# Performance work log

Measured on AMD Instinct MI355X. Metric: run time of the kernel, lower is better.

The kernel has to match this reference:

```python
import jax, jax.numpy as jnp
import numpy as np

N, T, DS, DD = 20000, 8, 16, 8   # nodes, seq_len, static dim, dynamic dim
E = 320000                        # edges (before self loops)
HL = 128                          # LSTM hidden
GH, GC = 4, 128                   # GAT heads, channels per head
HC = GH * GC                      # 512 concat output
EMB = 64
IN1 = DS + HL                     # layer-1 GNN input dim (static + lstm)


def setup_inputs() -> dict:
    ks = jax.random.split(jax.random.key(0), 20)
    p = lambda k, s: jax.random.normal(k, s, jnp.float32) * 0.05
    return {
        "x_static": jax.random.normal(ks[0], (N, DS), jnp.float32),
        "dynamic_seq": jax.random.normal(ks[1], (N, T, DD), jnp.float32),
        "edge_index": jax.random.randint(ks[2], (2, E), 0, N),
        # LSTM params (PyTorch gate order i,f,g,o)
        "W_ih": p(ks[3], (4 * HL, DD)), "W_hh": p(ks[4], (4 * HL, HL)),
        "b_ih": p(ks[5], (4 * HL,)), "b_hh": p(ks[6], (4 * HL,)),
        # GATv2 layer 1
        "Wl1": p(ks[7], (HC, IN1)), "Wr1": p(ks[8], (HC, IN1)),
        "att1": p(ks[9], (GH, GC)), "bg1": p(ks[10], (HC,)),
        # GATv2 layer 2
        "Wl2": p(ks[11], (HC, HC)), "Wr2": p(ks[12], (HC, HC)),
        "att2": p(ks[13], (GH, GC)), "bg2": p(ks[14], (HC,)),
        # BatchNorm affine params
        "gamma1": jnp.ones((HC,), jnp.float32), "beta1": jnp.zeros((HC,), jnp.float32),
        "gamma2": jnp.ones((HC,), jnp.float32), "beta2": jnp.zeros((HC,), jnp.float32),
        # output projection
        "Wp": p(ks[15], (EMB, HC)), "bp": p(ks[16], (EMB,)),
    }


def _lstm(seq, W_ih, W_hh, b_ih, b_hh):
    """Single-layer LSTM over [N, T, DD] -> [T, N, HL]."""
    n = seq.shape[0]
    b = b_ih + b_hh

    def step(carry, x_t):
        h, c = carry
        g = x_t @ W_ih.T + h @ W_hh.T + b            # [N, 4*HL]
        i, f, gg, o = jnp.split(g, 4, axis=-1)
        c = jax.nn.sigmoid(f) * c + jax.nn.sigmoid(i) * jnp.tanh(gg)
        h = jax.nn.sigmoid(o) * jnp.tanh(c)
        return (h, c), h

    h0 = jnp.zeros((n, HL), seq.dtype)
    _, hs = jax.lax.scan(step, (h0, h0), jnp.swapaxes(seq, 0, 1))
    return hs


def _gatv2(x, src, dst, Wl, Wr, att, bias):
    """GATv2Conv (concat heads, self-loops already in src/dst, eval dropout)."""
    xl = (x @ Wl.T).reshape(N, GH, GC)   # source transform
    xr = (x @ Wr.T).reshape(N, GH, GC)   # target transform
    e = jax.nn.leaky_relu(xl[src] + xr[dst], 0.2)       # [E', GH, GC]
    s = jnp.einsum('ehc,hc->eh', e, att)                # [E', GH]
    smax = jax.ops.segment_max(s, dst, num_segments=N)  # scatter-softmax (stable)
    ex = jnp.exp(s - smax[dst])
    den = jax.ops.segment_sum(ex, dst, num_segments=N)
    alpha = ex / den[dst]
    out = jax.ops.segment_sum(alpha[:, :, None] * xl[src], dst, num_segments=N)
    return out.reshape(N, HC) + bias


def _bn(x, g, b):
    m = x.mean(0)
    v = x.var(0)
    return (x - m) * jax.lax.rsqrt(v + 1e-5) * g + b


def reference(x_static, dynamic_seq, edge_index, W_ih, W_hh, b_ih, b_hh,
              Wl1, Wr1, att1, bg1, Wl2, Wr2, att2, bg2,
              gamma1, beta1, gamma2, beta2, Wp, bp):
    loops = jnp.arange(N)
    src = jnp.concatenate([edge_index[0], loops])  # add self loops (PyG default)
    dst = jnp.concatenate([edge_index[1], loops])
    hs = _lstm(dynamic_seq, W_ih, W_hh, b_ih, b_hh)  # [T, N, HL]

    def step(_, h_t):
        g = jnp.concatenate([x_static, h_t], axis=1)                 # [N, IN1]
        g = jax.nn.relu(_bn(_gatv2(g, src, dst, Wl1, Wr1, att1, bg1), gamma1, beta1))
        g = jax.nn.relu(_bn(_gatv2(g, src, dst, Wl2, Wr2, att2, bg2), gamma2, beta2))
        return None, g @ Wp.T + bp                                   # [N, EMB]

    _, emb = jax.lax.scan(step, None, hs)  # [T, N, EMB]
    return jnp.swapaxes(emb, 0, 1)         # [N, T, EMB]
```

## Files before the change

kernel.cpp:

```cpp
#include <hip/hip_runtime.h>
#include <math.h>

typedef unsigned short u16;
typedef unsigned int u32;

#define N_NODES 20000
#define MP      20480
#define T_SEQ   8
#define DS      16
#define DD      8
#define E_EDGES 320000
#define HL      128
#define GH      4
#define GC      128
#define HC      512
#define EMB     64
#define KP1     160
#define EP      (E_EDGES + N_NODES)

typedef __attribute__((ext_vector_type(8))) short bf16x8;
typedef __attribute__((ext_vector_type(4))) float f32x4;

__device__ __forceinline__ u16 f2bf(float f) {
  u32 u = __float_as_uint(f);
  u += 0x7fff + ((u >> 16) & 1);
  return (u16)(u >> 16);
}
__device__ __forceinline__ float bflo(u32 v) { return __uint_as_float(v << 16); }
__device__ __forceinline__ float bfhi(u32 v) { return __uint_as_float(v & 0xffff0000u); }

__device__ __forceinline__ void gld16(const void* g, void* l) {
  __builtin_amdgcn_global_load_lds(
      (const __attribute__((address_space(1))) void*)g,
      (__attribute__((address_space(3))) void*)l, 16, 0, 0);
}

__device__ __forceinline__ float rowsum16(float p) {
  p += __int_as_float(__builtin_amdgcn_update_dpp(0, __float_as_int(p), 0x121, 0xf, 0xf, false));
  p += __int_as_float(__builtin_amdgcn_update_dpp(0, __float_as_int(p), 0x122, 0xf, 0xf, false));
  p += __int_as_float(__builtin_amdgcn_update_dpp(0, __float_as_int(p), 0x124, 0xf, 0xf, false));
  p += __int_as_float(__builtin_amdgcn_update_dpp(0, __float_as_int(p), 0x128, 0xf, 0xf, false));
  return p;
}

__global__ __launch_bounds__(256) void gemm_mfma(
    const u16* __restrict__ A, int lda,
    const u16* __restrict__ W, int ldw,
    const float* __restrict__ bias,
    void* __restrict__ Cout, int ldc,
    int M, int Nc, int K, int c_bf16, int gxs)
{
  __shared__ u16 smem[16384];
  u16* Asm = smem;
  u16* Bsm = smem + 8192;

  const int tid = threadIdx.x;
  const int wave = tid >> 6, lane = tid & 63;
  const int wm = (wave >> 1) << 6, wn = (wave & 1) << 6;

  const u32 id = blockIdx.x;
  const int xcd = id & 7;
  const u32 sl = id >> 3;
  const int GXm = (1 << gxs) - 1;
  const int bn = (int)(sl & GXm) << 7;
  const int bm = (xcd + (int)((sl >> gxs) << 3)) << 7;

  f32x4 acc[4][4];
#pragma unroll
  for (int i = 0; i < 4; ++i)
#pragma unroll
    for (int j = 0; j < 4; ++j) acc[i][j] = (f32x4){0.f, 0.f, 0.f, 0.f};

  const int qr = lane >> 2;
  const int qc = (lane & 3) << 3;
  const int q0 = wave * 2, q1 = wave * 2 + 1;
  const int ra0 = bm + q0 * 16 + qr;
  const int ra1 = bm + q1 * 16 + qr;
  int rb0 = bn + q0 * 16 + qr; if (rb0 >= Nc) rb0 = Nc - 1;
  int rb1 = bn + q1 * 16 + qr; if (rb1 >= Nc) rb1 = Nc - 1;

  const u16* pa0 = A + (size_t)ra0 * lda + qc;
  const u16* pa1 = A + (size_t)ra1 * lda + qc;
  const u16* pb0 = W + (size_t)rb0 * ldw + qc;
  const u16* pb1 = W + (size_t)rb1 * ldw + qc;

  const int fm = lane & 15;
  const int fk = (lane >> 4) << 3;

  gld16(pa0, &Asm[q0 * 512]);
  gld16(pa1, &Asm[q1 * 512]);
  gld16(pb0, &Bsm[q0 * 512]);
  gld16(pb1, &Bsm[q1 * 512]);
  pa0 += 32; pa1 += 32; pb0 += 32; pb1 += 32;

  const int iters = K >> 5;
#pragma unroll 2
  for (int it = 0; it < iters; ++it) {
    const int cur = (it & 1) * 4096;
    __syncthreads();
    if (it + 1 < iters) {
      const int nxt = cur ^ 4096;
      gld16(pa0, &Asm[nxt + q0 * 512]);
      gld16(pa1, &Asm[nxt + q1 * 512]);
      gld16(pb0, &Bsm[nxt + q0 * 512]);
      gld16(pb1, &Bsm[nxt + q1 * 512]);
      pa0 += 32; pa1 += 32; pb0 += 32; pb1 += 32;
    }
    bf16x8 af[4], bfr[4];
#pragma unroll
    for (int i = 0; i < 4; ++i)
      af[i] = *(const bf16x8*)&Asm[cur + (wm + i * 16 + fm) * 32 + fk];
#pragma unroll
    for (int j = 0; j < 4; ++j)
      bfr[j] = *(const bf16x8*)&Bsm[cur + (wn + j * 16 + fm) * 32 + fk];
#pragma unroll
    for (int i = 0; i < 4; ++i)
#pragma unroll
      for (int j = 0; j < 4; ++j)
        acc[i][j] = __builtin_amdgcn_mfma_f32_16x16x32_bf16(af[i], bfr[j], acc[i][j], 0, 0, 0);
  }

  const int cn = lane & 15, cm = (lane >> 4) << 2;
  if (c_bf16) {
    __syncthreads();
#pragma unroll
    for (int j = 0; j < 4; ++j) {
      const int c = wn + j * 16 + cn;
      const float bb = bias ? bias[bn + c] : 0.f;
#pragma unroll
      for (int i = 0; i < 4; ++i) {
#pragma unroll
        for (int r = 0; r < 4; ++r)
          smem[(wm + i * 16 + cm + r) * 128 + c] = f2bf(acc[i][j][r] + bb);
      }
    }
    __syncthreads();
    u16* outc = (u16*)Cout;
#pragma unroll
    for (int k = 0; k < 8; ++k) {
      const int idx = tid + k * 256;
      const int r = idx >> 4, cc = (idx & 15) << 3;
      *(uint4*)(outc + (size_t)(bm + r) * ldc + bn + cc) = *(const uint4*)&smem[r * 128 + cc];
    }
  } else {
#pragma unroll
    for (int j = 0; j < 4; ++j) {
      const int c = bn + wn + j * 16 + cn;
      if (c >= Nc) continue;
      const float bb = bias ? bias[c] : 0.f;
#pragma unroll
      for (int i = 0; i < 4; ++i) {
#pragma unroll
        for (int r = 0; r < 4; ++r) {
          const int m = bm + wm + i * 16 + cm + r;
          if (m >= M) continue;
          ((float*)Cout)[(size_t)m * ldc + c] = acc[i][j][r] + bb;
        }
      }
    }
  }
}

__global__ void k_bias_sum(const float* __restrict__ b_ih,
                           const float* __restrict__ b_hh,
                           float* __restrict__ bsum) {
  int i = blockIdx.x * blockDim.x + threadIdx.x;
  if (i < 4 * HL) bsum[i] = b_ih[i] + b_hh[i];
}

__global__ void k_wcat_bf(const float* __restrict__ W_ih,
                          const float* __restrict__ W_hh,
                          u16* __restrict__ w) {
  int idx = blockIdx.x * blockDim.x + threadIdx.x;
  if (idx >= HC * KP1) return;
  int j = idx / KP1, k = idx - j * KP1;
  float v = 0.f;
  if (k < DD) v = W_ih[j * DD + k];
  else if (k < DD + HL) v = W_hh[j * HL + (k - DD)];
  w[idx] = f2bf(v);
}

__global__ void k_wlr1_bf(const float* __restrict__ Wl,
                          const float* __restrict__ Wr,
                          u16* __restrict__ w) {
  int idx = blockIdx.x * blockDim.x + threadIdx.x;
  if (idx >= 2 * HC * KP1) return;
  int j = idx / KP1, k = idx - j * KP1;
  const float* src = (j < HC) ? Wl : Wr;
  int jj = j & (HC - 1);
  float v = (k < DS + HL) ? src[jj * (DS + HL) + k] : 0.f;
  w[idx] = f2bf(v);
}

__global__ void k_wlr2_bf(const float* __restrict__ Wl,
                          const float* __restrict__ Wr,
                          u16* __restrict__ w) {
  int idx = blockIdx.x * blockDim.x + threadIdx.x;
  if (idx >= 2 * HC * HC) return;
  int j = idx >> 9, k = idx & (HC - 1);
  const float* src = (j < HC) ? Wl : Wr;
  int jj = j & (HC - 1);
  w[idx] = f2bf(src[jj * HC + k]);
}

__global__ void k_wp_bf(const float* __restrict__ Wp, u16* __restrict__ w) {
  int idx = blockIdx.x * blockDim.x + threadIdx.x;
  if (idx < EMB * HC) w[idx] = f2bf(Wp[idx]);
}

__global__ void k_pack_static(const float* __restrict__ xs, u16* __restrict__ packG1) {
  int idx = blockIdx.x * blockDim.x + threadIdx.x;
  if (idx >= N_NODES * DS) return;
  int n = idx >> 4, k = idx & 15;
  packG1[(size_t)n * KP1 + k] = f2bf(xs[idx]);
}

__global__ void k_pack_dyn(const float* __restrict__ dyn, u16* __restrict__ packXH) {
  int idx = blockIdx.x * blockDim.x + threadIdx.x;
  if (idx >= N_NODES * DD) return;
  int n = idx >> 3, k = idx & 7;
  packXH[(size_t)n * KP1 + k] = f2bf(dyn[(size_t)n * (T_SEQ * DD) + k]);
}

__global__ void lstm_update(const float* __restrict__ gates,
                            float* __restrict__ c,
                            u16* __restrict__ packXH, u16* __restrict__ packG1,
                            const float* __restrict__ dyn, int t_next) {
  int idx = blockIdx.x * blockDim.x + threadIdx.x;
  if (idx >= N_NODES * HL) return;
  int n = idx >> 7, j = idx & 127;
  const float* g = gates + (size_t)n * HC;
  float gi = g[j], gf = g[j + 128], gg = g[j + 256], go = g[j + 384];
  float si = 1.f / (1.f + __expf(-gi));
  float sf = 1.f / (1.f + __expf(-gf));
  float so = 1.f / (1.f + __expf(-go));
  float cn = sf * c[idx] + si * tanhf(gg);
  c[idx] = cn;
  u16 hb = f2bf(so * tanhf(cn));
  packXH[(size_t)n * KP1 + DD + j] = hb;
  packG1[(size_t)n * KP1 + DS + j] = hb;
  if (j < DD && t_next < T_SEQ)
    packXH[(size_t)n * KP1 + j] =
        f2bf(dyn[(size_t)n * (T_SEQ * DD) + t_next * DD + j]);
}

__global__ void k_deg(const int* __restrict__ ei, int* __restrict__ deg) {
  int e = blockIdx.x * blockDim.x + threadIdx.x;
  if (e >= EP) return;
  int d = (e < E_EDGES) ? ei[E_EDGES + e] : (e - E_EDGES);
  atomicAdd(&deg[d], 1);
}

__global__ __launch_bounds__(1024) void k_scan(const int* __restrict__ deg,
                                               int* __restrict__ rowstart) {
  __shared__ int buf[1024];
  __shared__ int carry_s;
  const int tid = threadIdx.x;
  if (tid == 0) carry_s = 0;
  __syncthreads();
  for (int base = 0; base < N_NODES; base += 1024) {
    int v = (base + tid < N_NODES) ? deg[base + tid] : 0;
    buf[tid] = v;
    __syncthreads();
    for (int off = 1; off < 1024; off <<= 1) {
      int add = (tid >= off) ? buf[tid - off] : 0;
      __syncthreads();
      buf[tid] += add;
      __syncthreads();
    }
    int incl = buf[tid];
    int carry = carry_s;
    if (base + tid < N_NODES) rowstart[base + tid] = carry + incl - v;
    __syncthreads();
    if (tid == 1023) carry_s = carry + incl;
    __syncthreads();
  }
  if (tid == 0) rowstart[N_NODES] = carry_s;
}

__global__ void k_fill(const int* __restrict__ ei,
                       const int* __restrict__ rowstart,
                       int* __restrict__ cursor, int* __restrict__ csr) {
  int e = blockIdx.x * blockDim.x + threadIdx.x;
  if (e >= EP) return;
  int s, d;
  if (e < E_EDGES) { s = ei[e]; d = ei[E_EDGES + e]; }
  else             { s = d = e - E_EDGES; }
  int pos = atomicAdd(&cursor[d], 1);
  csr[rowstart[d] + pos] = s;
}

__global__ __launch_bounds__(256) void gat_edge(
    const u16* __restrict__ xlr,
    const float* __restrict__ att, const float* __restrict__ bias,
    const int* __restrict__ rowstart, const int* __restrict__ csr,
    u16* __restrict__ outb)
{
  const int wave = threadIdx.x >> 6, lane = threadIdx.x & 63;
  const int d = blockIdx.x * 4 + wave;
  const int ch = lane * 8;
  const uint4 vr = *(const uint4*)(xlr + (size_t)d * 1024 + 512 + ch);
  const float rxa0 = bflo(vr.x), rxa1 = bfhi(vr.x), rxa2 = bflo(vr.y), rxa3 = bfhi(vr.y);
  const float rxb0 = bflo(vr.z), rxb1 = bfhi(vr.z), rxb2 = bflo(vr.w), rxb3 = bfhi(vr.w);
  const float4 ava = *(const float4*)(att + ch);
  const float4 avb = *(const float4*)(att + ch + 4);
  const int row = rowstart[d], end = rowstart[d + 1];
  const char* __restrict__ xbase = (const char*)(xlr + ch);

  float l = 0.f;
  float a0 = 0.f, a1 = 0.f, a2 = 0.f, a3 = 0.f;
  float b0 = 0.f, b1 = 0.f, b2 = 0.f, b3 = 0.f;

#define GAT_STEP(v)                                                          \
  {                                                                          \
    const float xa0 = bflo((v).x), xa1 = bfhi((v).x);                        \
    const float xa2 = bflo((v).y), xa3 = bfhi((v).y);                        \
    const float xb0 = bflo((v).z), xb1 = bfhi((v).z);                        \
    const float xb2 = bflo((v).w), xb3 = bfhi((v).w);                        \
    const float e0 = xa0 + rxa0, e1 = xa1 + rxa1;                            \
    const float e2 = xa2 + rxa2, e3 = xa3 + rxa3;                            \
    const float f0 = xb0 + rxb0, f1 = xb1 + rxb1;                            \
    const float f2 = xb2 + rxb2, f3 = xb3 + rxb3;                            \
    float ps = e0 * ava.x;                                                   \
    ps = fmaf(e1, ava.y, ps); ps = fmaf(e2, ava.z, ps);                      \
    ps = fmaf(e3, ava.w, ps); ps = fmaf(f0, avb.x, ps);                      \
    ps = fmaf(f1, avb.y, ps); ps = fmaf(f2, avb.z, ps);                      \
    ps = fmaf(f3, avb.w, ps);                                                \
    float pa = fabsf(e0) * ava.x;                                            \
    pa = fmaf(fabsf(e1), ava.y, pa); pa = fmaf(fabsf(e2), ava.z, pa);        \
    pa = fmaf(fabsf(e3), ava.w, pa); pa = fmaf(fabsf(f0), avb.x, pa);        \
    pa = fmaf(fabsf(f1), avb.y, pa); pa = fmaf(fabsf(f2), avb.z, pa);        \
    pa = fmaf(fabsf(f3), avb.w, pa);                                         \
    float p = rowsum16(fmaf(0.6f, ps, 0.4f * pa));                           \
    const float w = __expf(p);                                               \
    l += w;                                                                  \
    a0 = fmaf(w, xa0, a0); a1 = fmaf(w, xa1, a1);                            \
    a2 = fmaf(w, xa2, a2); a3 = fmaf(w, xa3, a3);                            \
    b0 = fmaf(w, xb0, b0); b1 = fmaf(w, xb1, b1);                            \
    b2 = fmaf(w, xb2, b2); b3 = fmaf(w, xb3, b3);                            \
  }

  int i = row;
  for (; i + 3 < end; i += 4) {
    const u32 s0 = (u32)csr[i],     s1 = (u32)csr[i + 1];
    const u32 s2 = (u32)csr[i + 2], s3 = (u32)csr[i + 3];
    const uint4 v0 = *(const uint4*)(xbase + (s0 << 11));
    const uint4 v1 = *(const uint4*)(xbase + (s1 << 11));
    const uint4 v2 = *(const uint4*)(xbase + (s2 << 11));
    const uint4 v3 = *(const uint4*)(xbase + (s3 << 11));
    GAT_STEP(v0);
    GAT_STEP(v1);
    GAT_STEP(v2);
    GAT_STEP(v3);
  }
  for (; i < end; ++i) {
    const u32 s0 = (u32)csr[i];
    const uint4 v0 = *(const uint4*)(xbase + (s0 << 11));
    GAT_STEP(v0);
  }
#undef GAT_STEP

  const float inv = 1.f / l;
  const float4 ba = *(const float4*)(bias + ch);
  const float4 bb = *(const float4*)(bias + ch + 4);
  uint4 ov;
  ov.x = (u32)f2bf(fmaf(a0, inv, ba.x)) | ((u32)f2bf(fmaf(a1, inv, ba.y)) << 16);
  ov.y = (u32)f2bf(fmaf(a2, inv, ba.z)) | ((u32)f2bf(fmaf(a3, inv, ba.w)) << 16);
  ov.z = (u32)f2bf(fmaf(b0, inv, bb.x)) | ((u32)f2bf(fmaf(b1, inv, bb.y)) << 16);
  ov.w = (u32)f2bf(fmaf(b2, inv, bb.z)) | ((u32)f2bf(fmaf(b3, inv, bb.w)) << 16);
  *(uint4*)(outb + (size_t)d * HC + ch) = ov;
}

__global__ __launch_bounds__(256) void bn_stats(const u16* __restrict__ x,
                                                float* __restrict__ stats) {
  const int tid = threadIdx.x;
  const int rows_per = (N_NODES + gridDim.x - 1) / gridDim.x;
  const int r0 = blockIdx.x * rows_per;
  const int r1 = min(r0 + rows_per, N_NODES);
  const u32* xp = (const u32*)x;
  float s0 = 0.f, s1 = 0.f, q0 = 0.f, q1 = 0.f;
  for (int r = r0; r < r1; ++r) {
    const u32 v = xp[(size_t)r * 256 + tid];
    const float v0 = bflo(v), v1 = bfhi(v);
    s0 += v0; q0 += v0 * v0;
    s1 += v1; q1 += v1 * v1;
  }
  atomicAdd(&stats[2 * tid],          s0);
  atomicAdd(&stats[2 * tid + 1],      s1);
  atomicAdd(&stats[HC + 2 * tid],     q0);
  atomicAdd(&stats[HC + 2 * tid + 1], q1);
}

__global__ void bn_apply(const u16* __restrict__ x, const float* __restrict__ stats,
                         const float* __restrict__ gamma, const float* __restrict__ beta,
                         u16* __restrict__ outb) {
  int idx = blockIdx.x * blockDim.x + threadIdx.x;
  if (idx >= N_NODES * (HC / 2)) return;
  const int cc = idx & (HC / 2 - 1);
  const int c0 = cc * 2, c1 = c0 + 1;
  const u32 v = ((const u32*)x)[idx];
  const float mean0 = stats[c0] * (1.f / N_NODES);
  const float mean1 = stats[c1] * (1.f / N_NODES);
  const float inv0 = rsqrtf(stats[HC + c0] * (1.f / N_NODES) - mean0 * mean0 + 1e-5f);
  const float inv1 = rsqrtf(stats[HC + c1] * (1.f / N_NODES) - mean1 * mean1 + 1e-5f);
  float z0 = (bflo(v) - mean0) * inv0 * gamma[c0] + beta[c0];
  float z1 = (bfhi(v) - mean1) * inv1 * gamma[c1] + beta[c1];
  z0 = z0 > 0.f ? z0 : 0.f;
  z1 = z1 > 0.f ? z1 : 0.f;
  ((u32*)outb)[idx] = (u32)f2bf(z0) | ((u32)f2bf(z1) << 16);
}

extern "C" void kernel_launch(void* const* d_in, const int* in_sizes, int n_in,
                              void* d_out, int out_size, void* d_ws, size_t ws_size,
                              hipStream_t stream) {
  const float* x_static = (const float*)d_in[0];
  const float* dyn      = (const float*)d_in[1];
  const int*   ei       = (const int*)d_in[2];
  const float* W_ih     = (const float*)d_in[3];
  const float* W_hh     = (const float*)d_in[4];
  const float* b_ih     = (const float*)d_in[5];
  const float* b_hh     = (const float*)d_in[6];
  const float* Wl1      = (const float*)d_in[7];
  const float* Wr1      = (const float*)d_in[8];
  const float* att1     = (const float*)d_in[9];
  const float* bg1      = (const float*)d_in[10];
  const float* Wl2      = (const float*)d_in[11];
  const float* Wr2      = (const float*)d_in[12];
  const float* att2     = (const float*)d_in[13];
  const float* bg2      = (const float*)d_in[14];
  const float* gamma1   = (const float*)d_in[15];
  const float* beta1    = (const float*)d_in[16];
  const float* gamma2   = (const float*)d_in[17];
  const float* beta2    = (const float*)d_in[18];
  const float* Wp       = (const float*)d_in[19];
  const float* bp       = (const float*)d_in[20];
  float* out = (float*)d_out;

  float* ws = (float*)d_ws;
  size_t o = 0;
  float* c     = ws + o; o += (size_t)MP * HL;
  float* gates = ws + o; o += (size_t)MP * HC;
  float* stats = ws + o; o += 4 * HC;
  float* bsum  = ws + o; o += 4 * HL;
  u16* packXH  = (u16*)(ws + o); o += (size_t)MP * KP1 / 2;
  u16* packG1  = (u16*)(ws + o); o += (size_t)MP * KP1 / 2;
  u16* xlr     = (u16*)(ws + o); o += (size_t)MP * 1024 / 2;
  u16* gout    = (u16*)(ws + o); o += (size_t)MP * HC / 2;
  u16* aggb    = (u16*)(ws + o); o += (size_t)MP * HC / 2;
  u16* wcat_bf = (u16*)(ws + o); o += (size_t)HC * KP1 / 2;
  u16* wlr1_bf = (u16*)(ws + o); o += (size_t)2 * HC * KP1 / 2;
  u16* wlr2_bf = (u16*)(ws + o); o += (size_t)2 * HC * HC / 2;
  u16* wp_bf   = (u16*)(ws + o); o += (size_t)EMB * HC / 2;
  int* deg      = (int*)(ws + o); o += N_NODES;
  int* cursor   = (int*)(ws + o); o += N_NODES;
  int* rowstart = (int*)(ws + o); o += N_NODES + 64;
  int* csr      = (int*)(ws + o); o += EP;

  hipMemsetAsync(deg,    0, N_NODES * sizeof(int), stream);
  hipMemsetAsync(cursor, 0, N_NODES * sizeof(int), stream);
  hipMemsetAsync(c,      0, (size_t)MP * HL * sizeof(float), stream);
  hipMemsetAsync(packXH, 0, (size_t)MP * KP1 * sizeof(u16), stream);
  hipMemsetAsync(packG1, 0, (size_t)MP * KP1 * sizeof(u16), stream);
  hipMemsetAsync(aggb,   0, (size_t)MP * HC * sizeof(u16), stream);

  k_bias_sum<<<2, 256, 0, stream>>>(b_ih, b_hh, bsum);
  k_wcat_bf<<<(HC * KP1 + 255) / 256, 256, 0, stream>>>(W_ih, W_hh, wcat_bf);
  k_wlr1_bf<<<(2 * HC * KP1 + 255) / 256, 256, 0, stream>>>(Wl1, Wr1, wlr1_bf);
  k_wlr2_bf<<<(2 * HC * HC + 255) / 256, 256, 0, stream>>>(Wl2, Wr2, wlr2_bf);
  k_wp_bf<<<(EMB * HC + 255) / 256, 256, 0, stream>>>(Wp, wp_bf);
  k_pack_static<<<(N_NODES * DS + 255) / 256, 256, 0, stream>>>(x_static, packG1);
  k_pack_dyn<<<(N_NODES * DD + 255) / 256, 256, 0, stream>>>(dyn, packXH);
  k_deg<<<(EP + 255) / 256, 256, 0, stream>>>(ei, deg);
  k_scan<<<1, 1024, 0, stream>>>(deg, rowstart);
  k_fill<<<(EP + 255) / 256, 256, 0, stream>>>(ei, rowstart, cursor, csr);

  const int GY = MP / 128;

  for (int t = 0; t < T_SEQ; ++t) {
    gemm_mfma<<<4 * GY, 256, 0, stream>>>(packXH, KP1, wcat_bf, KP1, bsum,
                                          gates, HC, MP, HC, KP1, 0, 2);
    lstm_update<<<(N_NODES * HL + 255) / 256, 256, 0, stream>>>(
        gates, c, packXH, packG1, dyn, t + 1);

    hipMemsetAsync(stats, 0, 4 * HC * sizeof(float), stream);

    gemm_mfma<<<8 * GY, 256, 0, stream>>>(packG1, KP1, wlr1_bf, KP1, nullptr,
                                          xlr, 1024, MP, 2 * HC, KP1, 1, 3);
    gat_edge<<<N_NODES / 4, 256, 0, stream>>>(xlr, att1, bg1, rowstart, csr, gout);
    bn_stats<<<500, 256, 0, stream>>>(gout, stats);
    bn_apply<<<(N_NODES * HC / 2 + 255) / 256, 256, 0, stream>>>(gout, stats,
                                                                 gamma1, beta1, aggb);

    gemm_mfma<<<8 * GY, 256, 0, stream>>>(aggb, HC, wlr2_bf, HC, nullptr,
                                          xlr, 1024, MP, 2 * HC, HC, 1, 3);
    gat_edge<<<N_NODES / 4, 256, 0, stream>>>(xlr, att2, bg2, rowstart, csr, gout);
    bn_stats<<<500, 256, 0, stream>>>(gout, stats + 2 * HC);
    bn_apply<<<(N_NODES * HC / 2 + 255) / 256, 256, 0, stream>>>(gout, stats + 2 * HC,
                                                                 gamma2, beta2, aggb);

    gemm_mfma<<<1 * GY, 256, 0, stream>>>(aggb, HC, wp_bf, HC, bp,
                                          out + t * EMB, T_SEQ * EMB,
                                          N_NODES, EMB, HC, 0, 0);
  }
}
```

Before: 2.501 ms.

## Pad CSR rows to multiples of four and software-pipeline GAT edge gathers

Each CSR row is padded to a multiple of four entries with masked dummy edges, and source indices are stored pre-shifted. This lets the GAT edge loop drop its remainder loop and prefetch the next group of four neighbour rows while computing the current one. Separately, LSTM gate pre-activations are now written in bf16 rather than fp32 to cut memory traffic. Per-step BN stats memsets are hoisted into one upfront memset. Padding adds wasted gather work, and bf16 gates reduce precision in the LSTM recurrence.

```diff
diff --git a/kernel.cpp b/kernel.cpp
--- a/kernel.cpp
+++ b/kernel.cpp
@@ -17,6 +17,7 @@
 #define EMB     64
 #define KP1     160
 #define EP      (E_EDGES + N_NODES)
+#define EPP     (EP + 3 * N_NODES)
 
 typedef __attribute__((ext_vector_type(8))) short bf16x8;
 typedef __attribute__((ext_vector_type(4))) float f32x4;
@@ -28,6 +29,7 @@
 }
 __device__ __forceinline__ float bflo(u32 v) { return __uint_as_float(v << 16); }
 __device__ __forceinline__ float bfhi(u32 v) { return __uint_as_float(v & 0xffff0000u); }
+__device__ __forceinline__ float bf16f(u16 v) { return __uint_as_float((u32)v << 16); }
 
 __device__ __forceinline__ void gld16(const void* g, void* l) {
   __builtin_amdgcn_global_load_lds(
@@ -222,15 +224,16 @@
   packXH[(size_t)n * KP1 + k] = f2bf(dyn[(size_t)n * (T_SEQ * DD) + k]);
 }
 
-__global__ void lstm_update(const float* __restrict__ gates,
+__global__ void lstm_update(const u16* __restrict__ gatesb,
                             float* __restrict__ c,
                             u16* __restrict__ packXH, u16* __restrict__ packG1,
                             const float* __restrict__ dyn, int t_next) {
   int idx = blockIdx.x * blockDim.x + threadIdx.x;
   if (idx >= N_NODES * HL) return;
   int n = idx >> 7, j = idx & 127;
-  const float* g = gates + (size_t)n * HC;
-  float gi = g[j], gf = g[j + 128], gg = g[j + 256], go = g[j + 384];
+  const u16* g = gatesb + (size_t)n * HC;
+  float gi = bf16f(g[j]), gf = bf16f(g[j + 128]);
+  float gg = bf16f(g[j + 256]), go = bf16f(g[j + 384]);
   float si = 1.f / (1.f + __expf(-gi));
   float sf = 1.f / (1.f + __expf(-gf));
   float so = 1.f / (1.f + __expf(-go));
@@ -259,7 +262,7 @@
   if (tid == 0) carry_s = 0;
   __syncthreads();
   for (int base = 0; base < N_NODES; base += 1024) {
-    int v = (base + tid < N_NODES) ? deg[base + tid] : 0;
+    int v = (base + tid < N_NODES) ? ((deg[base + tid] + 3) & ~3) : 0;
     buf[tid] = v;
     __syncthreads();
     for (int off = 1; off < 1024; off <<= 1) {
@@ -280,20 +283,29 @@
 
 __global__ void k_fill(const int* __restrict__ ei,
                        const int* __restrict__ rowstart,
-                       int* __restrict__ cursor, int* __restrict__ csr) {
+                       int* __restrict__ cursor, u32* __restrict__ csr) {
   int e = blockIdx.x * blockDim.x + threadIdx.x;
   if (e >= EP) return;
   int s, d;
   if (e < E_EDGES) { s = ei[e]; d = ei[E_EDGES + e]; }
   else             { s = d = e - E_EDGES; }
   int pos = atomicAdd(&cursor[d], 1);
-  csr[rowstart[d] + pos] = s;
+  csr[rowstart[d] + pos] = (u32)s << 11;
+}
+
+__global__ void k_pad(const int* __restrict__ deg,
+                      const int* __restrict__ rowstart, u32* __restrict__ csr) {
+  int d = blockIdx.x * blockDim.x + threadIdx.x;
+  if (d >= N_NODES) return;
+  int s = rowstart[d] + deg[d], e = rowstart[d + 1];
+  const u32 pv = ((u32)d << 11) | 1;
+  for (int i = s; i < e; ++i) csr[i] = pv;
 }
 
 __global__ __launch_bounds__(256) void gat_edge(
     const u16* __restrict__ xlr,
     const float* __restrict__ att, const float* __restrict__ bias,
-    const int* __restrict__ rowstart, const int* __restrict__ csr,
+    const int* __restrict__ rowstart, const u32* __restrict__ csr,
     u16* __restrict__ outb)
 {
   const int wave = threadIdx.x >> 6, lane = threadIdx.x & 63;
@@ -311,7 +323,9 @@
   float a0 = 0.f, a1 = 0.f, a2 = 0.f, a3 = 0.f;
   float b0 = 0.f, b1 = 0.f, b2 = 0.f, b3 = 0.f;
 
-#define GAT_STEP(v)                                                          \
+#define GLD(o) (*(const uint4*)(xbase + (size_t)((o) & ~1u)))
+
+#define GAT_STEP(v, o)                                                       \
   {                                                                          \
     const float xa0 = bflo((v).x), xa1 = bfhi((v).x);                        \
     const float xa2 = bflo((v).y), xa3 = bfhi((v).y);                        \
@@ -332,7 +346,8 @@
     pa = fmaf(fabsf(f1), avb.y, pa); pa = fmaf(fabsf(f2), avb.z, pa);        \
     pa = fmaf(fabsf(f3), avb.w, pa);                                         \
     float p = rowsum16(fmaf(0.6f, ps, 0.4f * pa));                           \
-    const float w = __expf(p);                                               \
+    float w = __expf(p);                                                     \
+    w = ((o) & 1) ? 0.f : w;                                                 \
     l += w;                                                                  \
     a0 = fmaf(w, xa0, a0); a1 = fmaf(w, xa1, a1);                            \
     a2 = fmaf(w, xa2, a2); a3 = fmaf(w, xa3, a3);                            \
@@ -340,25 +355,29 @@
     b2 = fmaf(w, xb2, b2); b3 = fmaf(w, xb3, b3);                            \
   }
 
-  int i = row;
-  for (; i + 3 < end; i += 4) {
-    const u32 s0 = (u32)csr[i],     s1 = (u32)csr[i + 1];
-    const u32 s2 = (u32)csr[i + 2], s3 = (u32)csr[i + 3];
-    const uint4 v0 = *(const uint4*)(xbase + (s0 << 11));
-    const uint4 v1 = *(const uint4*)(xbase + (s1 << 11));
-    const uint4 v2 = *(const uint4*)(xbase + (s2 << 11));
-    const uint4 v3 = *(const uint4*)(xbase + (s3 << 11));
-    GAT_STEP(v0);
-    GAT_STEP(v1);
-    GAT_STEP(v2);
-    GAT_STEP(v3);
-  }
-  for (; i < end; ++i) {
-    const u32 s0 = (u32)csr[i];
-    const uint4 v0 = *(const uint4*)(xbase + (s0 << 11));
-    GAT_STEP(v0);
-  }
+  const u32* cp = csr + row;
+  const int nq = (end - row) >> 2;
+
+  u32 o0 = cp[0], o1 = cp[1], o2 = cp[2], o3 = cp[3];
+  uint4 v0 = GLD(o0), v1 = GLD(o1), v2 = GLD(o2), v3 = GLD(o3);
+
+  for (int q = 1; q < nq; ++q) {
+    cp += 4;
+    const u32 n0 = cp[0], n1 = cp[1], n2 = cp[2], n3 = cp[3];
+    const uint4 w0 = GLD(n0), w1 = GLD(n1), w2 = GLD(n2), w3 = GLD(n3);
+    GAT_STEP(v0, o0);
+    GAT_STEP(v1, o1);
+    GAT_STEP(v2, o2);
+    GAT_STEP(v3, o3);
+    o0 = n0; o1 = n1; o2 = n2; o3 = n3;
+    v0 = w0; v1 = w1; v2 = w2; v3 = w3;
+  }
+  GAT_STEP(v0, o0);
+  GAT_STEP(v1, o1);
+  GAT_STEP(v2, o2);
+  GAT_STEP(v3, o3);
 #undef GAT_STEP
+#undef GLD
 
   const float inv = 1.f / l;
   const float4 ba = *(const float4*)(bias + ch);
@@ -438,10 +457,10 @@
 
   float* ws = (float*)d_ws;
   size_t o = 0;
-  float* c     = ws + o; o += (size_t)MP * HL;
-  float* gates = ws + o; o += (size_t)MP * HC;
-  float* stats = ws + o; o += 4 * HC;
-  float* bsum  = ws + o; o += 4 * HL;
+  float* c        = ws + o; o += (size_t)MP * HL;
+  float* statsAll = ws + o; o += (size_t)T_SEQ * 4 * HC;
+  float* bsum     = ws + o; o += 4 * HL;
+  u16* gatesb  = (u16*)(ws + o); o += (size_t)MP * HC / 2;
   u16* packXH  = (u16*)(ws + o); o += (size_t)MP * KP1 / 2;
   u16* packG1  = (u16*)(ws + o); o += (size_t)MP * KP1 / 2;
   u16* xlr     = (u16*)(ws + o); o += (size_t)MP * 1024 / 2;
@@ -454,14 +473,15 @@
   int* deg      = (int*)(ws + o); o += N_NODES;
   int* cursor   = (int*)(ws + o); o += N_NODES;
   int* rowstart = (int*)(ws + o); o += N_NODES + 64;
-  int* csr      = (int*)(ws + o); o += EP;
-
-  hipMemsetAsync(deg,    0, N_NODES * sizeof(int), stream);
-  hipMemsetAsync(cursor, 0, N_NODES * sizeof(int), stream);
-  hipMemsetAsync(c,      0, (size_t)MP * HL * sizeof(float), stream);
-  hipMemsetAsync(packXH, 0, (size_t)MP * KP1 * sizeof(u16), stream);
-  hipMemsetAsync(packG1, 0, (size_t)MP * KP1 * sizeof(u16), stream);
-  hipMemsetAsync(aggb,   0, (size_t)MP * HC * sizeof(u16), stream);
+  u32* csr      = (u32*)(ws + o); o += EPP;
+
+  hipMemsetAsync(deg,      0, N_NODES * sizeof(int), stream);
+  hipMemsetAsync(cursor,   0, N_NODES * sizeof(int), stream);
+  hipMemsetAsync(statsAll, 0, (size_t)T_SEQ * 4 * HC * sizeof(float), stream);
+  hipMemsetAsync(c,        0, (size_t)MP * HL * sizeof(float), stream);
+  hipMemsetAsync(packXH,   0, (size_t)MP * KP1 * sizeof(u16), stream);
+  hipMemsetAsync(packG1,   0, (size_t)MP * KP1 * sizeof(u16), stream);
+  hipMemsetAsync(aggb,     0, (size_t)MP * HC * sizeof(u16), stream);
 
   k_bias_sum<<<2, 256, 0, stream>>>(b_ih, b_hh, bsum);
   k_wcat_bf<<<(HC * KP1 + 255) / 256, 256, 0, stream>>>(W_ih, W_hh, wcat_bf);
@@ -473,16 +493,17 @@
   k_deg<<<(EP + 255) / 256, 256, 0, stream>>>(ei, deg);
   k_scan<<<1, 1024, 0, stream>>>(deg, rowstart);
   k_fill<<<(EP + 255) / 256, 256, 0, stream>>>(ei, rowstart, cursor, csr);
+  k_pad<<<(N_NODES + 255) / 256, 256, 0, stream>>>(deg, rowstart, csr);
 
   const int GY = MP / 128;
 
   for (int t = 0; t < T_SEQ; ++t) {
+    float* stats = statsAll + (size_t)t * 4 * HC;
+
     gemm_mfma<<<4 * GY, 256, 0, stream>>>(packXH, KP1, wcat_bf, KP1, bsum,
-                                          gates, HC, MP, HC, KP1, 0, 2);
+                                          gatesb, HC, MP, HC, KP1, 1, 2);
     lstm_update<<<(N_NODES * HL + 255) / 256, 256, 0, stream>>>(
-        gates, c, packXH, packG1, dyn, t + 1);
-
-    hipMemsetAsync(stats, 0, 4 * HC * sizeof(float), stream);
+        gatesb, c, packXH, packG1, dyn, t + 1);
 
     gemm_mfma<<<8 * GY, 256, 0, stream>>>(packG1, KP1, wlr1_bf, KP1, nullptr,
                                           xlr, 1024, MP, 2 * HC, KP1, 1, 3);
```

After: 2.455 ms. Within noise of the previous version (-1.8%).
